# Optimization experiments

Hardware: AMD Instinct MI355X
Metric: run time of the kernel (lower is better)

The kernel has to match this reference:

```python
import jax, jax.numpy as jnp
import numpy as np

ENCODER_DIM = 2048
DECODER_DIM = 512
ATTENTION_DIM = 512
BATCH = 512
NUM_PIXELS = 196


def setup_inputs() -> dict:
    key = jax.random.key(0)
    k = jax.random.split(key, 8)
    s_e = 1.0 / np.sqrt(ENCODER_DIM)
    s_d = 1.0 / np.sqrt(DECODER_DIM)
    s_a = 1.0 / np.sqrt(ATTENTION_DIM)
    return {
        "encoder_out": jax.random.normal(k[0], (BATCH, NUM_PIXELS, ENCODER_DIM), jnp.float32),
        "decoder_hidden": jax.random.normal(k[1], (BATCH, DECODER_DIM), jnp.float32),
        "W_enc": jax.random.uniform(k[2], (ENCODER_DIM, ATTENTION_DIM), jnp.float32, -s_e, s_e),
        "b_enc": jax.random.uniform(k[3], (ATTENTION_DIM,), jnp.float32, -s_e, s_e),
        "W_dec": jax.random.uniform(k[4], (DECODER_DIM, ATTENTION_DIM), jnp.float32, -s_d, s_d),
        "b_dec": jax.random.uniform(k[5], (ATTENTION_DIM,), jnp.float32, -s_d, s_d),
        "W_full": jax.random.uniform(k[6], (ATTENTION_DIM,), jnp.float32, -s_a, s_a),
        "b_full": jax.random.uniform(k[7], (), jnp.float32, -s_a, s_a),
    }


def reference(encoder_out, decoder_hidden, W_enc, b_enc, W_dec, b_dec, W_full, b_full):
    # att1: [B, P, A], att2: [B, A]
    att1 = jnp.einsum('bpe,ea->bpa', encoder_out, W_enc) + b_enc
    att2 = decoder_hidden @ W_dec + b_dec
    # scores: [B, P]
    scores = jnp.einsum('bpa,a->bp', jnp.tanh(att1 + att2[:, None, :]), W_full) + b_full
    alpha = jax.nn.softmax(scores, axis=1)
    context = jnp.einsum('bpe,bp->be', encoder_out, alpha)
    return context, alpha
```

## Files before the change

### kernel.cpp

```cpp
#include <hip/hip_runtime.h>
#include <hip/hip_bf16.h>
#include <stdint.h>

#define BATCH 512
#define PIX   196
#define EDIM  2048
#define DDIM  512
#define ADIM  512
#define MROWS (BATCH*PIX)

#define BM 256
#define BN 256
#define BK 64
#define NT (EDIM/BK)

typedef __attribute__((ext_vector_type(8))) short bf16x8;
typedef __attribute__((ext_vector_type(8))) float f32x8;
typedef __attribute__((ext_vector_type(8))) __bf16 bf16v8;
typedef __attribute__((ext_vector_type(4))) float f32x4;

#define GLL16(g, lptr) __builtin_amdgcn_global_load_lds( \
    (const __attribute__((address_space(1))) void*)(g),  \
    (__attribute__((address_space(3))) void*)(lptr), 16, 0, 0)

static __device__ __forceinline__ unsigned short f2bf(float f) {
  union { float f; uint32_t u; } v; v.f = f;
  uint32_t u = v.u;
  return (unsigned short)((u + 0x7FFFu + ((u >> 16) & 1u)) >> 16);
}

static __device__ __forceinline__ bf16x8 cvt8(float4 a, float4 b) {
  f32x8 v = {a.x, a.y, a.z, a.w, b.x, b.y, b.z, b.w};
  bf16v8 c = __builtin_convertvector(v, bf16v8);
  bf16x8 r;
  __builtin_memcpy(&r, &c, 16);
  return r;
}

__global__ void k_transpose_wenc(const float* __restrict__ W,
                                 unsigned short* __restrict__ Bt) {
  __shared__ float tile[32][33];
  const int kt = blockIdx.x;
  const int nt = blockIdx.y;
  const int tx = threadIdx.x, ty = threadIdx.y;
#pragma unroll
  for (int j = 0; j < 4; j++)
    tile[ty + 8*j][tx] = W[(size_t)(kt*32 + ty + 8*j)*ADIM + nt*32 + tx];
  __syncthreads();
#pragma unroll
  for (int j = 0; j < 4; j++)
    Bt[(size_t)(nt*32 + ty + 8*j)*EDIM + kt*32 + tx] = f2bf(tile[tx][ty + 8*j]);
}

__global__ void k_att2(const float* __restrict__ H, const float* __restrict__ Wd,
                       const float* __restrict__ bd, float* __restrict__ att2) {
  __shared__ float h[DDIM];
  const int b = blockIdx.x;
  const int t = threadIdx.x;
  h[t]       = H[(size_t)b*DDIM + t];
  h[t + 256] = H[(size_t)b*DDIM + t + 256];
  __syncthreads();
  float a0 = 0.f, a1 = 0.f;
#pragma unroll 8
  for (int k = 0; k < DDIM; k++) {
    const float hv = h[k];
    a0 += hv * Wd[(size_t)k*ADIM + t];
    a1 += hv * Wd[(size_t)k*ADIM + t + 256];
  }
  att2[(size_t)b*ADIM + t]       = a0 + bd[t];
  att2[(size_t)b*ADIM + t + 256] = a1 + bd[t + 256];
}

__global__ __launch_bounds__(512) void k_gemm_scores(
    const float* __restrict__ enc,
    const unsigned short* __restrict__ Bt,
    const float* __restrict__ b_enc,
    const float* __restrict__ att2,
    const float* __restrict__ W_full,
    float* __restrict__ scores)
{
  __shared__ __align__(16) char ldsA[2*32768];
  __shared__ __align__(16) char ldsB[2*32768];
  __shared__ float sc[BM];

  const int t   = threadIdx.x;
  const int l   = t & 63;
  const int wid = t >> 6;
  const int wr  = wid >> 2;
  const int wc  = wid & 3;

  const int orig = blockIdx.x;
  const int tile = (orig & 7) * 98 + (orig >> 3);
  const int bm0 = (tile >> 1) * BM;
  const int bn0 = (tile & 1) * BN;

  if (t < BM) sc[t] = 0.f;

  const int arow = t >> 1;
  const int ah   = t & 1;
  const float* srcA = enc + (size_t)(bm0 + arow) * EDIM + ah * 32;
  int wA[4];
#pragma unroll
  for (int j = 0; j < 4; j++)
    wA[j] = arow*128 + (((ah*4 + j) ^ (arow & 7)) * 16);

  const unsigned short* srcB[4];
#pragma unroll
  for (int j = 0; j < 4; j++) {
    const int row = (t >> 3) + j*64;
    srcB[j] = Bt + (size_t)(bn0 + row) * EDIM + ((t & 7) ^ (row & 7)) * 8;
  }
  const int dstB = wid * 1024;

  const int l15 = l & 15, hi = l >> 4;
  const int sw  = l15 & 7;
  const int c0  = (hi ^ sw) * 16;
  const int c1  = ((4 + hi) ^ sw) * 16;
  const int baseA = (wr*128 + l15) * 128;
  const int baseB = (wc*64  + l15) * 128;

  float4 ar[8];
  f32x4 acc[8][4] = {};

#define A_ISSUE(KT) do {                                         \
    const float* _s = srcA + (size_t)(KT) * BK;                  \
    _Pragma("unroll")                                            \
    for (int j = 0; j < 8; j++) ar[j] = ((const float4*)_s)[j];  \
  } while (0)

#define B_GLL(NXT, KT) do {                                      \
    _Pragma("unroll")                                            \
    for (int j = 0; j < 4; j++)                                  \
      GLL16(srcB[j] + (size_t)(KT) * BK,                         \
            ldsB + (NXT)*32768 + dstB + j*8192);                 \
  } while (0)

#define A_WRITE(NXT) do {                                        \
    _Pragma("unroll")                                            \
    for (int j = 0; j < 4; j++) {                                \
      bf16x8 w = cvt8(ar[2*j], ar[2*j + 1]);                     \
      *(bf16x8*)(ldsA + (NXT)*32768 + wA[j]) = w;                \
    }                                                            \
  } while (0)

#define COMPUTE(CUR) do {                                        \
    _Pragma("unroll")                                            \
    for (int ks = 0; ks < 2; ks++) {                             \
      const int cks = ks ? c1 : c0;                              \
      bf16x8 bfr[4], af[8];                                      \
      _Pragma("unroll")                                          \
      for (int ni = 0; ni < 4; ni++)                             \
        bfr[ni] = *(const bf16x8*)(ldsB + (CUR)*32768 + baseB + ni*2048 + cks); \
      _Pragma("unroll")                                          \
      for (int mi = 0; mi < 8; mi++)                             \
        af[mi] = *(const bf16x8*)(ldsA + (CUR)*32768 + baseA + mi*2048 + cks);  \
      __builtin_amdgcn_s_setprio(1);                             \
      _Pragma("unroll")                                          \
      for (int mi = 0; mi < 8; mi++)                             \
        _Pragma("unroll")                                        \
        for (int ni = 0; ni < 4; ni++)                           \
          acc[mi][ni] = __builtin_amdgcn_mfma_f32_16x16x32_bf16( \
              af[mi], bfr[ni], acc[mi][ni], 0, 0, 0);            \
      __builtin_amdgcn_s_setprio(0);                             \
    }                                                            \
  } while (0)

#define ITER(KT, CUR, NXT, DO_STAGE) do {                        \
    if (DO_STAGE) { A_ISSUE((KT)+1); B_GLL(NXT, (KT)+1); }       \
    COMPUTE(CUR);                                                \
    if (DO_STAGE) {                                              \
      asm volatile("s_waitcnt vmcnt(4)" ::: "memory");           \
      A_WRITE(NXT);                                              \
    }                                                            \
    asm volatile("s_waitcnt vmcnt(0) lgkmcnt(0)" ::: "memory");  \
    __builtin_amdgcn_s_barrier();                                \
  } while (0)

  A_ISSUE(0);
  B_GLL(0, 0);
  asm volatile("s_waitcnt vmcnt(4)" ::: "memory");
  A_WRITE(0);
  asm volatile("s_waitcnt vmcnt(0) lgkmcnt(0)" ::: "memory");
  __builtin_amdgcn_s_barrier();

  for (int kb = 0; kb < NT - 2; kb += 2) {
    ITER(kb,     0, 1, true);
    ITER(kb + 1, 1, 0, true);
  }
  ITER(NT - 2, 0, 1, true);
  COMPUTE(1);

  float be[4], wf[4];
  int colv[4];
#pragma unroll
  for (int ni = 0; ni < 4; ni++) {
    colv[ni] = bn0 + wc*64 + ni*16 + l15;
    be[ni] = b_enc[colv[ni]];
    wf[ni] = W_full[colv[ni]];
  }
#pragma unroll
  for (int mi = 0; mi < 8; mi++) {
#pragma unroll
    for (int e = 0; e < 4; e++) {
      const int row_l = wr*128 + mi*16 + hi*4 + e;
      const unsigned gr = (unsigned)(bm0 + row_l);
      const unsigned b  = gr / 196u;
      float s = 0.f;
#pragma unroll
      for (int ni = 0; ni < 4; ni++) {
        const float v = acc[mi][ni][e] + be[ni] + att2[(size_t)b*ADIM + colv[ni]];
        s += tanhf(v) * wf[ni];
      }
      s += __shfl_xor(s, 1); s += __shfl_xor(s, 2);
      s += __shfl_xor(s, 4); s += __shfl_xor(s, 8);
      if (l15 == 0) atomicAdd(&sc[row_l], s);
    }
  }
  __syncthreads();
  if (t < BM) atomicAdd(&scores[bm0 + t], sc[t]);
}

__global__ void k_softmax(float* __restrict__ sa) {
  __shared__ float red[256];
  const int b = blockIdx.x, t = threadIdx.x;
  const float v = (t < PIX) ? sa[(size_t)b*PIX + t] : -1e30f;
  red[t] = v; __syncthreads();
  for (int s2 = 128; s2 > 0; s2 >>= 1) {
    if (t < s2) red[t] = fmaxf(red[t], red[t + s2]);
    __syncthreads();
  }
  const float m = red[0]; __syncthreads();
  const float e = (t < PIX) ? __expf(v - m) : 0.f;
  red[t] = e; __syncthreads();
  for (int s2 = 128; s2 > 0; s2 >>= 1) {
    if (t < s2) red[t] += red[t + s2];
    __syncthreads();
  }
  const float inv = 1.f / red[0];
  if (t < PIX) sa[(size_t)b*PIX + t] = e * inv;
}

__global__ __launch_bounds__(512) void k_context(
    const float* __restrict__ enc, const float* __restrict__ alpha,
    float* __restrict__ ctx) {
  __shared__ float al[PIX];
  const int b = blockIdx.x, t = threadIdx.x;
  if (t < PIX) al[t] = alpha[(size_t)b*PIX + t];
  __syncthreads();
  const float4* e4 = (const float4*)(enc + (size_t)b * PIX * EDIM);
  float4 acc = {0.f, 0.f, 0.f, 0.f};
#pragma unroll 4
  for (int p = 0; p < PIX; p++) {
    const float4 v = e4[(size_t)p * (EDIM/4) + t];
    const float a = al[p];
    acc.x += v.x * a; acc.y += v.y * a; acc.z += v.z * a; acc.w += v.w * a;
  }
  ((float4*)(ctx + (size_t)b * EDIM))[t] = acc;
}

extern "C" void kernel_launch(void* const* d_in, const int* in_sizes, int n_in,
                              void* d_out, int out_size, void* d_ws, size_t ws_size,
                              hipStream_t stream) {
  (void)in_sizes; (void)n_in; (void)out_size; (void)ws_size;
  const float* enc   = (const float*)d_in[0];
  const float* hid   = (const float*)d_in[1];
  const float* Wenc  = (const float*)d_in[2];
  const float* benc  = (const float*)d_in[3];
  const float* Wdec  = (const float*)d_in[4];
  const float* bdec  = (const float*)d_in[5];
  const float* Wfull = (const float*)d_in[6];

  unsigned short* Bt = (unsigned short*)d_ws;
  float* att2 = (float*)((char*)d_ws + (size_t)ADIM * EDIM * 2);
  float* ctx   = (float*)d_out;
  float* alpha = (float*)d_out + (size_t)BATCH * EDIM;

  hipMemsetAsync(alpha, 0, (size_t)MROWS * sizeof(float), stream);
  k_transpose_wenc<<<dim3(64, 16), dim3(32, 8), 0, stream>>>(Wenc, Bt);
  k_att2<<<BATCH, 256, 0, stream>>>(hid, Wdec, bdec, att2);
  k_gemm_scores<<<784, 512, 0, stream>>>(enc, Bt, benc, att2, Wfull, alpha);
  k_softmax<<<BATCH, 256, 0, stream>>>(alpha);
  k_context<<<BATCH, 512, 0, stream>>>(enc, alpha, ctx);
}
```

Baseline: 710.8 us.

## Split each K-tile into four barrier-fenced phases interleaving loads with MFMA

Restructures the main GEMM loop into four sub-phases per K tile, each issuing part of the next tile's global loads and LDS reads, then a barrier-synchronized block of 16 MFMAs at raised priority. The aim is to interleave memory traffic with matrix math across waves (ping-pong style) and shrink the fragment register footprint (af drops from 8 to 4). In exchange it adds many more workgroup barriers per tile, which can stall waves if phases are unbalanced.

```diff
diff --git a/kernel.cpp b/kernel.cpp
--- a/kernel.cpp
+++ b/kernel.cpp
@@ -120,6 +120,7 @@
   const int baseB = (wc*64  + l15) * 128;
 
   float4 ar[8];
+  bf16x8 af[4], bfr[4];
   f32x4 acc[8][4] = {};
 
 #define A_ISSUE(KT) do {                                         \
@@ -128,12 +129,8 @@
     for (int j = 0; j < 8; j++) ar[j] = ((const float4*)_s)[j];  \
   } while (0)
 
-#define B_GLL(NXT, KT) do {                                      \
-    _Pragma("unroll")                                            \
-    for (int j = 0; j < 4; j++)                                  \
-      GLL16(srcB[j] + (size_t)(KT) * BK,                         \
-            ldsB + (NXT)*32768 + dstB + j*8192);                 \
-  } while (0)
+#define B_GLLJ(NXT, KT, J) \
+    GLL16(srcB[J] + (size_t)(KT) * BK, ldsB + (NXT)*32768 + dstB + (J)*8192)
 
 #define A_WRITE(NXT) do {                                        \
     _Pragma("unroll")                                            \
@@ -143,52 +140,81 @@
     }                                                            \
   } while (0)
 
-#define COMPUTE(CUR) do {                                        \
-    _Pragma("unroll")                                            \
-    for (int ks = 0; ks < 2; ks++) {                             \
-      const int cks = ks ? c1 : c0;                              \
-      bf16x8 bfr[4], af[8];                                      \
+#define DSREAD_B(CUR, CKS) do {                                  \
+    _Pragma("unroll")                                            \
+    for (int ni = 0; ni < 4; ni++)                               \
+      bfr[ni] = *(const bf16x8*)(ldsB + (CUR)*32768 + baseB + ni*2048 + (CKS)); \
+  } while (0)
+
+#define DSREAD_A(CUR, CKS, MOFF) do {                            \
+    _Pragma("unroll")                                            \
+    for (int mi = 0; mi < 4; mi++)                               \
+      af[mi] = *(const bf16x8*)(ldsA + (CUR)*32768 + baseA + (mi+(MOFF))*2048 + (CKS)); \
+  } while (0)
+
+#define BARLG()                                                  \
+    __builtin_amdgcn_s_barrier();                                \
+    asm volatile("s_waitcnt lgkmcnt(0)" ::: "memory");           \
+    __builtin_amdgcn_sched_barrier(0);                           \
+    __builtin_amdgcn_s_setprio(1)
+
+#define ENDBAR()                                                 \
+    __builtin_amdgcn_s_setprio(0);                               \
+    __builtin_amdgcn_s_barrier()
+
+#define MF16(MOFF) do {                                          \
+    _Pragma("unroll")                                            \
+    for (int mi = 0; mi < 4; mi++)                               \
       _Pragma("unroll")                                          \
       for (int ni = 0; ni < 4; ni++)                             \
-        bfr[ni] = *(const bf16x8*)(ldsB + (CUR)*32768 + baseB + ni*2048 + cks); \
-      _Pragma("unroll")                                          \
-      for (int mi = 0; mi < 8; mi++)                             \
-        af[mi] = *(const bf16x8*)(ldsA + (CUR)*32768 + baseA + mi*2048 + cks);  \
-      __builtin_amdgcn_s_setprio(1);                             \
-      _Pragma("unroll")                                          \
-      for (int mi = 0; mi < 8; mi++)                             \
-        _Pragma("unroll")                                        \
-        for (int ni = 0; ni < 4; ni++)                           \
-          acc[mi][ni] = __builtin_amdgcn_mfma_f32_16x16x32_bf16( \
-              af[mi], bfr[ni], acc[mi][ni], 0, 0, 0);            \
-      __builtin_amdgcn_s_setprio(0);                             \
-    }                                                            \
-  } while (0)
-
-#define ITER(KT, CUR, NXT, DO_STAGE) do {                        \
-    if (DO_STAGE) { A_ISSUE((KT)+1); B_GLL(NXT, (KT)+1); }       \
-    COMPUTE(CUR);                                                \
-    if (DO_STAGE) {                                              \
-      asm volatile("s_waitcnt vmcnt(4)" ::: "memory");           \
-      A_WRITE(NXT);                                              \
-    }                                                            \
-    asm volatile("s_waitcnt vmcnt(0) lgkmcnt(0)" ::: "memory");  \
-    __builtin_amdgcn_s_barrier();                                \
+        acc[mi+(MOFF)][ni] = __builtin_amdgcn_mfma_f32_16x16x32_bf16( \
+            af[mi], bfr[ni], acc[mi+(MOFF)][ni], 0, 0, 0);       \
+  } while (0)
+
+#define TILE(KT, CUR, NXT) do {                                  \
+                                                         \
+    A_ISSUE((KT)+1);                                             \
+    DSREAD_B(CUR, c0); DSREAD_A(CUR, c0, 0);                     \
+    BARLG(); MF16(0); ENDBAR();                                  \
+                                                         \
+    B_GLLJ(NXT, (KT)+1, 0); B_GLLJ(NXT, (KT)+1, 1);              \
+    DSREAD_A(CUR, c0, 4);                                        \
+    BARLG(); MF16(4); ENDBAR();                                  \
+                                                         \
+    B_GLLJ(NXT, (KT)+1, 2); B_GLLJ(NXT, (KT)+1, 3);              \
+    DSREAD_B(CUR, c1); DSREAD_A(CUR, c1, 0);                     \
+    BARLG(); MF16(0); ENDBAR();                                  \
+                                                         \
+    asm volatile("s_waitcnt vmcnt(4)" ::: "memory");             \
+    A_WRITE(NXT);                                                \
+    DSREAD_A(CUR, c1, 4);                                        \
+    BARLG(); MF16(4);                                            \
+    asm volatile("s_waitcnt vmcnt(0)" ::: "memory");             \
+    ENDBAR();                                                    \
   } while (0)
 
   A_ISSUE(0);
-  B_GLL(0, 0);
+  B_GLLJ(0, 0, 0); B_GLLJ(0, 0, 1); B_GLLJ(0, 0, 2); B_GLLJ(0, 0, 3);
   asm volatile("s_waitcnt vmcnt(4)" ::: "memory");
   A_WRITE(0);
   asm volatile("s_waitcnt vmcnt(0) lgkmcnt(0)" ::: "memory");
   __builtin_amdgcn_s_barrier();
 
-  for (int kb = 0; kb < NT - 2; kb += 2) {
-    ITER(kb,     0, 1, true);
-    ITER(kb + 1, 1, 0, true);
-  }
-  ITER(NT - 2, 0, 1, true);
-  COMPUTE(1);
+  for (int kb = 0; kb < 30; kb += 2) {
+    TILE(kb,     0, 1);
+    TILE(kb + 1, 1, 0);
+  }
+  TILE(30, 0, 1);
+
+#pragma unroll
+  for (int ks = 0; ks < 2; ks++) {
+    const int cks = ks ? c1 : c0;
+    DSREAD_B(1, cks);
+    DSREAD_A(1, cks, 0);
+    MF16(0);
+    DSREAD_A(1, cks, 4);
+    MF16(4);
+  }
 
   float be[4], wf[4];
   int colv[4];
```

Measured after the change: 734.4 us. +3.3%, slower.
